# Kernel optimization log

Hardware: AMD Instinct MI355X
Metric: run time of the kernel (lower is better)

## Reference

```python
import jax, jax.numpy as jnp
import numpy as np

B, N, F, T, O, E = 4, 30000, 32, 12, 64, 480000


def setup_inputs() -> dict:
    key = jax.random.key(0)
    ks = jax.random.split(key, 20)
    s = 0.05
    inp = {
        "X": jax.random.normal(ks[0], (B, N, F, T), dtype=jnp.float32),
        "edge_index": jax.random.randint(ks[1], (2, E), 0, N, dtype=jnp.int64),
        # GCNConv weights for the three gates (num_layers=1 -> single conv each)
        "Wg_z": jax.random.normal(ks[2], (F, O), dtype=jnp.float32) * s,
        "bg_z": jnp.zeros((O,), jnp.float32),
        "Wg_r": jax.random.normal(ks[3], (F, O), dtype=jnp.float32) * s,
        "bg_r": jnp.zeros((O,), jnp.float32),
        "Wg_h": jax.random.normal(ks[4], (F, O), dtype=jnp.float32) * s,
        "bg_h": jnp.zeros((O,), jnp.float32),
        # gate Linear(2*O, O) weights
        "Wl_z": jax.random.normal(ks[5], (2 * O, O), dtype=jnp.float32) * s,
        "bl_z": jnp.zeros((O,), jnp.float32),
        "Wl_r": jax.random.normal(ks[6], (2 * O, O), dtype=jnp.float32) * s,
        "bl_r": jnp.zeros((O,), jnp.float32),
        "Wl_h": jax.random.normal(ks[7], (2 * O, O), dtype=jnp.float32) * s,
        "bl_h": jnp.zeros((O,), jnp.float32),
        # A3TGCN per-period attention and final readout Linear(O, T)
        "att": jax.random.normal(ks[8], (T,), dtype=jnp.float32),
        "W_out": jax.random.normal(ks[9], (O, T), dtype=jnp.float32) * s,
        "b_out": jnp.zeros((T,), jnp.float32),
    }
    return inp


def reference(X, edge_index, Wg_z, bg_z, Wg_r, bg_r, Wg_h, bg_h,
              Wl_z, bl_z, Wl_r, bl_r, Wl_h, bl_h, att, W_out, b_out):
    src, dst = edge_index[0], edge_index[1]
    n = X.shape[1]
    # GCN symmetric normalization with self-loops: deg = in-degree + 1
    deg = jnp.zeros((n,), X.dtype).at[dst].add(1.0) + 1.0
    dis = jax.lax.rsqrt(deg)  # deg^{-1/2}
    edge_norm = (dis[src] * dis[dst])[None, :, None]  # [1,E,1]
    self_norm = (dis * dis)[None, :, None]            # [1,N,1]

    def gcn_conv(x, W, b):  # x: [B,N,F] -> [B,N,O]
        xw = jnp.einsum('bnf,fo->bno', x, W)
        agg = jnp.zeros_like(xw).at[:, dst, :].add(xw[:, src, :] * edge_norm)
        return agg + xw * self_norm + b

    H0 = jnp.zeros((X.shape[0], n, Wg_z.shape[1]), X.dtype)  # H defaults to zeros
    probs = jax.nn.softmax(att)

    def step(acc, inp):
        x_t, p = inp  # x_t: [B,N,F]
        Z = jax.nn.sigmoid(jnp.concatenate([gcn_conv(x_t, Wg_z, bg_z), H0], -1) @ Wl_z + bl_z)
        R = jax.nn.sigmoid(jnp.concatenate([gcn_conv(x_t, Wg_r, bg_r), H0], -1) @ Wl_r + bl_r)
        Ht = jnp.tanh(jnp.concatenate([gcn_conv(x_t, Wg_h, bg_h), H0 * R], -1) @ Wl_h + bl_h)
        Hn = Z * H0 + (1.0 - Z) * Ht
        return acc + p * Hn, None

    Xt = jnp.moveaxis(X, -1, 0)  # [T,B,N,F]
    H_acc, _ = jax.lax.scan(step, jnp.zeros_like(H0), (Xt, probs))
    # TemporalGNN head: ReLU + Linear(O, periods)
    return jax.nn.relu(H_acc) @ W_out + b_out  # [B,N,T]
```

## Files before the change

kernel.cpp:

```cpp
#include <hip/hip_runtime.h>
#include <hip/hip_bf16.h>
#include <hip/hip_fp16.h>


#define FDIM 32
#define TDIM 12
#define ODIM 64
#define BDIM 4
#define SCAN_TILE 1024

typedef _Float16 half8v __attribute__((ext_vector_type(8)));
typedef float float4v __attribute__((ext_vector_type(4)));

__global__ __launch_bounds__(256) void kA(
    const float4* __restrict__ Xin, uint2* __restrict__ Xh, int n4, int cvtB,
    const int* __restrict__ dstE, int* __restrict__ counts, int E, int cntB,
    const float* __restrict__ Wg_z, const float* __restrict__ bg_z,
    const float* __restrict__ Wl_z, const float* __restrict__ bl_z,
    const float* __restrict__ Wg_h, const float* __restrict__ bg_h,
    const float* __restrict__ Wl_h, const float* __restrict__ bl_h,
    const float* __restrict__ att,
    float* __restrict__ Wz, float* __restrict__ bz,
    float* __restrict__ Wh, float* __restrict__ bh,
    float* __restrict__ probs) {
    const int bid = blockIdx.x;
    const int tid = threadIdx.x;
    if (bid < cvtB) {
        int i = bid * 256 + tid;
        const int stride = cvtB * 256;
        for (; i < n4; i += stride) {
            const float4 v = Xin[i];
            __half2 h0 = __floats2half2_rn(v.x, v.y);
            __half2 h1 = __floats2half2_rn(v.z, v.w);
            uint2 u;
            u.x = *reinterpret_cast<unsigned*>(&h0);
            u.y = *reinterpret_cast<unsigned*>(&h1);
            Xh[i] = u;
        }
    } else if (bid < cvtB + cntB) {
        int e = (bid - cvtB) * 256 + tid;
        if (e < E) atomicAdd(&counts[dstE[e]], 1);
    } else {
        for (int i = tid; i < FDIM * ODIM; i += 256) {
            int f = i >> 6, o = i & 63;
            float az = 0.f, ah = 0.f;
            for (int k = 0; k < ODIM; k++) {
                az += Wg_z[f * ODIM + k] * Wl_z[k * ODIM + o];
                ah += Wg_h[f * ODIM + k] * Wl_h[k * ODIM + o];
            }
            Wz[i] = az;
            Wh[i] = ah;
        }
        if (tid < ODIM) {
            float az = bl_z[tid], ah = bl_h[tid];
            for (int k = 0; k < ODIM; k++) {
                az += bg_z[k] * Wl_z[k * ODIM + tid];
                ah += bg_h[k] * Wl_h[k * ODIM + tid];
            }
            bz[tid] = az;
            bh[tid] = ah;
        }
        if (tid == 0) {
            float m = -1e30f;
            for (int t = 0; t < TDIM; t++) m = fmaxf(m, att[t]);
            float e[TDIM], s = 0.f;
            for (int t = 0; t < TDIM; t++) { e[t] = expf(att[t] - m); s += e[t]; }
            for (int t = 0; t < TDIM; t++) probs[t] = e[t] / s;
        }
    }
}

__global__ __launch_bounds__(256) void kB1(const int* __restrict__ counts, int N,
                                           int* __restrict__ partials) {
    __shared__ int wsum[4];
    const int tid = threadIdx.x;
    const int blk = blockIdx.x;
    const int i0 = blk * SCAN_TILE + tid * 4;
    int s = 0;
    s += (i0 + 0 < N) ? counts[i0 + 0] + 1 : 0;
    s += (i0 + 1 < N) ? counts[i0 + 1] + 1 : 0;
    s += (i0 + 2 < N) ? counts[i0 + 2] + 1 : 0;
    s += (i0 + 3 < N) ? counts[i0 + 3] + 1 : 0;
    for (int off = 1; off < 64; off <<= 1) s += __shfl_xor(s, off, 64);
    if ((tid & 63) == 0) wsum[tid >> 6] = s;
    __syncthreads();
    if (tid == 0) partials[blk] = wsum[0] + wsum[1] + wsum[2] + wsum[3];
}

__global__ __launch_bounds__(256) void kB3(const int* __restrict__ counts, int N,
                                           const int* __restrict__ partials,
                                           int* __restrict__ offsets,
                                           float* __restrict__ dis,
                                           int* __restrict__ fill,
                                           int2* __restrict__ csr, int E) {
    __shared__ int sBase;
    __shared__ int wsum[4];
    const int tid = threadIdx.x;
    const int blk = blockIdx.x;
    const int lane = tid & 63;
    const int wv = tid >> 6;

    if (tid == 0) {
        int acc = 0;
        for (int j = 0; j < blk; j++) acc += partials[j];
        sBase = acc;
    }

    const int i0 = blk * SCAN_TILE + tid * 4;
    const int e0 = (i0 + 0 < N) ? counts[i0 + 0] + 1 : 0;
    const int e1 = (i0 + 1 < N) ? counts[i0 + 1] + 1 : 0;
    const int e2 = (i0 + 2 < N) ? counts[i0 + 2] + 1 : 0;
    const int e3 = (i0 + 3 < N) ? counts[i0 + 3] + 1 : 0;
    const int s = e0 + e1 + e2 + e3;
    int inc = s;
    for (int off = 1; off < 64; off <<= 1) {
        int t = __shfl_up(inc, off, 64);
        if (lane >= off) inc += t;
    }
    if (lane == 63) wsum[wv] = inc;
    __syncthreads();
    int wbase = 0;
    for (int j = 0; j < wv; j++) wbase += wsum[j];
    int base = sBase + wbase + inc - s;

    const int ee[4] = {e0, e1, e2, e3};
#pragma unroll
    for (int k = 0; k < 4; k++) {
        const int i = i0 + k;
        if (i < N) {
            offsets[i] = base;
            const float d = 1.0f / sqrtf((float)ee[k]);
            dis[i] = d;
            fill[i] = 1;
            const float nm = d * d;
            __half2 mh = __floats2half2_rn(nm, nm);
            csr[base] = make_int2(i, *(int*)&mh);
            base += ee[k];
        }
    }
    if (blk == 0 && tid == 0) offsets[N] = E + N;
}

__global__ void k_scatter(const int* __restrict__ src, const int* __restrict__ dst,
                          const int* __restrict__ offsets, int* __restrict__ fill,
                          const float* __restrict__ dis,
                          int2* __restrict__ csr, int E) {
    int e = blockIdx.x * 256 + threadIdx.x;
    if (e < E) {
        int s = src[e], d = dst[e];
        int pos = offsets[d] + atomicAdd(&fill[d], 1);
        float nm = dis[s] * dis[d];
        __half2 mh = __floats2half2_rn(nm, nm);
        csr[pos] = make_int2(s, *(int*)&mh);
    }
}

__device__ __forceinline__ float sigm(float x) { return 1.f / (1.f + __expf(-x)); }
__device__ __forceinline__ float tanhfast(float x) { return 1.f - 2.f / (1.f + __expf(2.f * x)); }

#define HPACC(mhI, v, hs0, hs1, hs2, hs3)                                      \
    {                                                                          \
        int mi_ = (mhI);                                                       \
        __half2 mh_ = *(__half2*)&mi_;                                         \
        hs0 = __hfma2(mh_, *(__half2*)&(v).x, hs0);                            \
        hs1 = __hfma2(mh_, *(__half2*)&(v).y, hs1);                            \
        hs2 = __hfma2(mh_, *(__half2*)&(v).z, hs2);                            \
        hs3 = __hfma2(mh_, *(__half2*)&(v).w, hs3);                            \
    }

#define HFLUSH(hs0, hs1, hs2, hs3)                                             \
    {                                                                          \
        float2 t_;                                                             \
        t_ = __half22float2(hs0); a0 += t_.x; a1 += t_.y;                      \
        t_ = __half22float2(hs1); a2 += t_.x; a3 += t_.y;                      \
        t_ = __half22float2(hs2); a4 += t_.x; a5 += t_.y;                      \
        t_ = __half22float2(hs3); a6 += t_.x; a7 += t_.y;                      \
        hs0 = hzero; hs1 = hzero; hs2 = hzero; hs3 = hzero;                    \
    }

#define LOADB(dst, Wsrc, jt)                                                   \
    {                                                                          \
        _Pragma("unroll") for (int r_ = 0; r_ < 8; r_++)                       \
            dst[r_] = (_Float16)Wsrc[(kg * 8 + r_) * ODIM + (jt) * 16 + c];    \
    }

#define EPI(qv, dzv, dhv, bzv, bhv)                                            \
    {                                                                          \
        float s_ = 0.f;                                                        \
        {  const float zf_ = dzv[0] + bzv, hf_ = dhv[0] + bhv;                 \
           const float u_ = __expf(-zf_), v_ = __expf(2.f * hf_);              \
           s_ += pr0 * u_ * (v_ - 1.f) *                                       \
                 __builtin_amdgcn_rcpf((1.f + u_) * (1.f + v_)); }             \
        {  const float zf_ = dzv[1] + bzv, hf_ = dhv[1] + bhv;                 \
           const float u_ = __expf(-zf_), v_ = __expf(2.f * hf_);              \
           s_ += pr1 * u_ * (v_ - 1.f) *                                       \
                 __builtin_amdgcn_rcpf((1.f + u_) * (1.f + v_)); }             \
        {  const float zf_ = dzv[2] + bzv, hf_ = dhv[2] + bhv;                 \
           const float u_ = __expf(-zf_), v_ = __expf(2.f * hf_);              \
           s_ += pr2 * u_ * (v_ - 1.f) *                                       \
                 __builtin_amdgcn_rcpf((1.f + u_) * (1.f + v_)); }             \
        {  const float zf_ = dzv[3] + bzv, hf_ = dhv[3] + bhv;                 \
           const float u_ = __expf(-zf_), v_ = __expf(2.f * hf_);              \
           s_ += pr3 * u_ * (v_ - 1.f) *                                       \
                 __builtin_amdgcn_rcpf((1.f + u_) * (1.f + v_)); }             \
        s_ += __shfl_xor(s_, 16, 64);                                          \
        s_ += __shfl_xor(s_, 32, 64);                                          \
        qv = s_;                                                               \
    }

__global__ __launch_bounds__(256, 4) void k_main_w(
    const uint4* __restrict__ Xh, const int* __restrict__ offs,
    const int2* __restrict__ csr,
    const float* __restrict__ Wz, const float* __restrict__ bz,
    const float* __restrict__ Wh, const float* __restrict__ bh,
    const float* __restrict__ probs, const float* __restrict__ Wout,
    const float* __restrict__ bout, float* __restrict__ out, int N) {
    __shared__ float sY[4][16 * 36 + 4];

    const int tid = threadIdx.x;
    const int wv = tid >> 6;
    const int lane = tid & 63;
    const int lanec = lane < 47 ? lane : 47;
    const int c = lane & 15;
    const int kg = lane >> 4;

    half8v wzf0, wzf1, wzf2, wzf3, whf0, whf1, whf2, whf3;
    LOADB(wzf0, Wz, 0) LOADB(wzf1, Wz, 1) LOADB(wzf2, Wz, 2) LOADB(wzf3, Wz, 3)
    LOADB(whf0, Wh, 0) LOADB(whf1, Wh, 1) LOADB(whf2, Wh, 2) LOADB(whf3, Wh, 3)
    half8v wo0, wo1;
#pragma unroll
    for (int r_ = 0; r_ < 8; r_++) {
        wo0[r_] = (_Float16)((c < TDIM) ? Wout[(kg * 8 + r_) * TDIM + c] : 0.f);
        wo1[r_] = (_Float16)((c < TDIM) ? Wout[(32 + kg * 8 + r_) * TDIM + c] : 0.f);
    }
    const float bz0 = bz[c], bz1 = bz[16 + c], bz2 = bz[32 + c], bz3 = bz[48 + c];
    const float bh0 = bh[c], bh1 = bh[16 + c], bh2 = bh[32 + c], bh3 = bh[48 + c];
    const float pr0 = (kg * 4 + 0 < TDIM) ? probs[kg * 4 + 0] : 0.f;
    const float pr1 = (kg * 4 + 1 < TDIM) ? probs[kg * 4 + 1] : 0.f;
    const float pr2 = (kg * 4 + 2 < TDIM) ? probs[kg * 4 + 2] : 0.f;
    const float pr3 = (kg * 4 + 3 < TDIM) ? probs[kg * 4 + 3] : 0.f;
    const float bo = (lane < TDIM) ? bout[lane] : 0.f;
    const __half2 hzero = __float2half2_rn(0.f);

    float* __restrict__ sy = sY[wv];
    const int strideT = gridDim.x * 4;
    const int totalTasks = N * BDIM;

    int task0 = blockIdx.x * 4 + wv;
    if (task0 >= totalTasks) return;
    int b = task0 / N;
    int n = task0 - b * N;

    while (true) {
        const int bs = __builtin_amdgcn_readfirstlane(b);
        const int ns = __builtin_amdgcn_readfirstlane(n);
        const unsigned rowB = (unsigned)bs * (unsigned)N;
        const int begS = __builtin_amdgcn_readfirstlane(offs[ns]);
        const int endS = __builtin_amdgcn_readfirstlane(offs[ns + 1]);

        float a0 = 0.f, a1 = 0.f, a2 = 0.f, a3 = 0.f,
              a4 = 0.f, a5 = 0.f, a6 = 0.f, a7 = 0.f;
        __half2 hA0 = hzero, hA1 = hzero, hA2 = hzero, hA3 = hzero;
        __half2 hB0 = hzero, hB1 = hzero, hB2 = hzero, hB3 = hzero;
        int j = begS;
        for (; j + 8 <= endS; j += 8) {
            const int2 e0 = csr[j + 0], e1 = csr[j + 1], e2 = csr[j + 2], e3 = csr[j + 3];
            const int2 e4 = csr[j + 4], e5 = csr[j + 5], e6 = csr[j + 6], e7 = csr[j + 7];
            const uint4 x0 = Xh[(rowB + (unsigned)e0.x) * 48u + lanec];
            const uint4 x1 = Xh[(rowB + (unsigned)e1.x) * 48u + lanec];
            const uint4 x2 = Xh[(rowB + (unsigned)e2.x) * 48u + lanec];
            const uint4 x3 = Xh[(rowB + (unsigned)e3.x) * 48u + lanec];
            const uint4 x4 = Xh[(rowB + (unsigned)e4.x) * 48u + lanec];
            const uint4 x5 = Xh[(rowB + (unsigned)e5.x) * 48u + lanec];
            const uint4 x6 = Xh[(rowB + (unsigned)e6.x) * 48u + lanec];
            const uint4 x7 = Xh[(rowB + (unsigned)e7.x) * 48u + lanec];
            HPACC(e0.y, x0, hA0, hA1, hA2, hA3);
            HPACC(e1.y, x1, hA0, hA1, hA2, hA3);
            HPACC(e2.y, x2, hA0, hA1, hA2, hA3);
            HPACC(e3.y, x3, hA0, hA1, hA2, hA3);
            HPACC(e4.y, x4, hB0, hB1, hB2, hB3);
            HPACC(e5.y, x5, hB0, hB1, hB2, hB3);
            HPACC(e6.y, x6, hB0, hB1, hB2, hB3);
            HPACC(e7.y, x7, hB0, hB1, hB2, hB3);
            HFLUSH(hA0, hA1, hA2, hA3);
            HFLUSH(hB0, hB1, hB2, hB3);
        }
        for (; j < endS; ++j) {
            const int2 e = csr[j];
            const uint4 xv = Xh[(rowB + (unsigned)e.x) * 48u + lanec];
            HPACC(e.y, xv, hA0, hA1, hA2, hA3);
        }
        HFLUSH(hA0, hA1, hA2, hA3);

        if (lane < 48) {
            int flat = lane * 8;
            int f = flat / 12;
            int t = flat - f * 12;
#pragma unroll
            for (int k = 0; k < 8; k++) {
                float av = (k == 0) ? a0 : (k == 1) ? a1 : (k == 2) ? a2 :
                           (k == 3) ? a3 : (k == 4) ? a4 : (k == 5) ? a5 :
                           (k == 6) ? a6 : a7;
                sy[t * 36 + f] = av;
                t++;
                if (t == TDIM) { t = 0; f++; }
            }
        }

        half8v af;
        if (c < TDIM) {
            const float4* yp = (const float4*)&sy[c * 36 + kg * 8];
            const float4 y0 = yp[0];
            const float4 y1 = yp[1];
            af[0] = (_Float16)y0.x; af[1] = (_Float16)y0.y;
            af[2] = (_Float16)y0.z; af[3] = (_Float16)y0.w;
            af[4] = (_Float16)y1.x; af[5] = (_Float16)y1.y;
            af[6] = (_Float16)y1.z; af[7] = (_Float16)y1.w;
        } else {
            af[0] = (_Float16)0.f; af[1] = (_Float16)0.f;
            af[2] = (_Float16)0.f; af[3] = (_Float16)0.f;
            af[4] = (_Float16)0.f; af[5] = (_Float16)0.f;
            af[6] = (_Float16)0.f; af[7] = (_Float16)0.f;
        }

        const float4v zero4 = {0.f, 0.f, 0.f, 0.f};
        float4v dz0 = __builtin_amdgcn_mfma_f32_16x16x32_f16(af, wzf0, zero4, 0, 0, 0);
        float4v dz1 = __builtin_amdgcn_mfma_f32_16x16x32_f16(af, wzf1, zero4, 0, 0, 0);
        float4v dz2 = __builtin_amdgcn_mfma_f32_16x16x32_f16(af, wzf2, zero4, 0, 0, 0);
        float4v dz3 = __builtin_amdgcn_mfma_f32_16x16x32_f16(af, wzf3, zero4, 0, 0, 0);
        float4v dh0 = __builtin_amdgcn_mfma_f32_16x16x32_f16(af, whf0, zero4, 0, 0, 0);
        float4v dh1 = __builtin_amdgcn_mfma_f32_16x16x32_f16(af, whf1, zero4, 0, 0, 0);
        float4v dh2 = __builtin_amdgcn_mfma_f32_16x16x32_f16(af, whf2, zero4, 0, 0, 0);
        float4v dh3 = __builtin_amdgcn_mfma_f32_16x16x32_f16(af, whf3, zero4, 0, 0, 0);

        float q0, q1, q2, q3;
        EPI(q0, dz0, dh0, bz0, bh0)
        EPI(q1, dz1, dh1, bz1, bh1)
        EPI(q2, dz2, dh2, bz2, bh2)
        EPI(q3, dz3, dh3, bz3, bh3)
        const float accOwn = (kg == 0) ? q0 : (kg == 1) ? q1 : (kg == 2) ? q2 : q3;

        const float r = fmaxf(accOwn, 0.f);
        half8v ra0, ra1;
#pragma unroll
        for (int j2 = 0; j2 < 8; j2++) {
            ra0[j2] = (_Float16)__shfl(r, (kg << 3) + j2, 64);
            ra1[j2] = (_Float16)__shfl(r, 32 + (kg << 3) + j2, 64);
        }
        float4v dro = __builtin_amdgcn_mfma_f32_16x16x32_f16(ra0, wo0, zero4, 0, 0, 0);
        dro = __builtin_amdgcn_mfma_f32_16x16x32_f16(ra1, wo1, dro, 0, 0, 0);
        if (lane < TDIM)
            out[(rowB + (unsigned)n) * TDIM + lane] = dro[0] + bo;

        n += strideT;
        if (n >= N) { n -= N; b++; }
        if (b >= BDIM) break;
    }
}

__global__ __launch_bounds__(384) void k_main_f(
    const float* __restrict__ X, const int* __restrict__ offsets,
    const int2* __restrict__ csr, const float* __restrict__ dis,
    const float* __restrict__ Wz, const float* __restrict__ bz,
    const float* __restrict__ Wh, const float* __restrict__ bh,
    const float* __restrict__ probs, const float* __restrict__ Wout,
    const float* __restrict__ bout, float* __restrict__ out, int N) {
    const int tid = threadIdx.x;
    const int lane = tid & 63;

    __shared__ float4 sY4[BDIM][96];
    __shared__ float sAcc[BDIM][ODIM];
    __shared__ float sWout[ODIM * TDIM];
    __shared__ float sBout[TDIM];

    for (int i = tid; i < ODIM * TDIM; i += 384) sWout[i] = Wout[i];
    if (tid < TDIM) sBout[tid] = bout[tid];

    const int o = tid & 63;
    const int w = tid >> 6;
    float wzr[FDIM], whr[FDIM];
#pragma unroll
    for (int f = 0; f < FDIM; f++) {
        wzr[f] = Wz[f * ODIM + o];
        whr[f] = Wh[f * ODIM + o];
    }
    const float bzo = bz[o], bho = bh[o];
    const int t0 = w, t1 = w + 6;
    const float p0 = probs[t0], p1 = probs[t1];

    const int b = tid / 96;
    const int q = tid - b * 96;
    const float4* __restrict__ Xq = (const float4*)X;
    const unsigned rowBase = (unsigned)b * (unsigned)N;

    for (int n = blockIdx.x; n < N; n += gridDim.x) {
        if (tid < BDIM * ODIM) ((float*)sAcc)[tid] = 0.f;

        const int beg = offsets[n], end = offsets[n + 1];
        float4 A0 = make_float4(0.f, 0.f, 0.f, 0.f);
        float4 A1 = A0, A2 = A0, A3 = A0;

        for (int ebase = beg; ebase < end; ebase += 64) {
            const int cnt2 = min(64, end - ebase);
            int esrc = 0;
            float enm = 0.f;
            if (ebase + lane < end) {
                const int2 e = csr[ebase + lane];
                esrc = e.x;
                int ey = e.y;
                enm = __half22float2(*(__half2*)&ey).x;
            }
            int j = 0;
            for (; j + 4 <= cnt2; j += 4) {
                const int s0 = __shfl(esrc, j + 0, 64), s1 = __shfl(esrc, j + 1, 64);
                const int s2 = __shfl(esrc, j + 2, 64), s3 = __shfl(esrc, j + 3, 64);
                const float m0 = __shfl(enm, j + 0, 64), m1 = __shfl(enm, j + 1, 64);
                const float m2 = __shfl(enm, j + 2, 64), m3 = __shfl(enm, j + 3, 64);
                const float4 u0 = Xq[(rowBase + s0) * 96u + q];
                const float4 u1 = Xq[(rowBase + s1) * 96u + q];
                const float4 u2 = Xq[(rowBase + s2) * 96u + q];
                const float4 u3 = Xq[(rowBase + s3) * 96u + q];
                A0.x += m0 * u0.x; A0.y += m0 * u0.y; A0.z += m0 * u0.z; A0.w += m0 * u0.w;
                A1.x += m1 * u1.x; A1.y += m1 * u1.y; A1.z += m1 * u1.z; A1.w += m1 * u1.w;
                A2.x += m2 * u2.x; A2.y += m2 * u2.y; A2.z += m2 * u2.z; A2.w += m2 * u2.w;
                A3.x += m3 * u3.x; A3.y += m3 * u3.y; A3.z += m3 * u3.z; A3.w += m3 * u3.w;
            }
            for (; j < cnt2; j++) {
                const int s = __shfl(esrc, j, 64);
                const float m = __shfl(enm, j, 64);
                const float4 u = Xq[(rowBase + s) * 96u + q];
                A0.x += m * u.x; A0.y += m * u.y; A0.z += m * u.z; A0.w += m * u.w;
            }
        }
        A0.x += (A1.x + A2.x) + A3.x;
        A0.y += (A1.y + A2.y) + A3.y;
        A0.z += (A1.z + A2.z) + A3.z;
        A0.w += (A1.w + A2.w) + A3.w;
        sY4[b][q] = A0;
        __syncthreads();

#pragma unroll
        for (int bb = 0; bb < BDIM; bb++) {
            const float* yb = (const float*)sY4[bb];
            float z0 = bzo, z1 = bzo, h0 = bho, h1 = bho;
#pragma unroll
            for (int f = 0; f < FDIM; f++) {
                float ya = yb[f * TDIM + t0];
                float yc = yb[f * TDIM + t1];
                z0 += ya * wzr[f]; h0 += ya * whr[f];
                z1 += yc * wzr[f]; h1 += yc * whr[f];
            }
            float contrib = p0 * (1.f - sigm(z0)) * tanhfast(h0)
                          + p1 * (1.f - sigm(z1)) * tanhfast(h1);
            atomicAdd(&sAcc[bb][o], contrib);
        }
        __syncthreads();

        if (tid < BDIM * TDIM) {
            int ob = tid / TDIM, jj = tid - ob * TDIM;
            float v = sBout[jj];
#pragma unroll
            for (int o2 = 0; o2 < ODIM; o2++) {
                v += fmaxf(sAcc[ob][o2], 0.f) * sWout[o2 * TDIM + jj];
            }
            out[(unsigned)(ob * N + n) * TDIM + jj] = v;
        }
        __syncthreads();
    }
}

extern "C" void kernel_launch(void* const* d_in, const int* in_sizes, int n_in,
                              void* d_out, int out_size, void* d_ws, size_t ws_size,
                              hipStream_t stream) {
    const float* X    = (const float*)d_in[0];
    const int*   ei   = (const int*)d_in[1];
    const float* Wg_z = (const float*)d_in[2];
    const float* bg_z = (const float*)d_in[3];
    const float* Wg_h = (const float*)d_in[6];
    const float* bg_h = (const float*)d_in[7];
    const float* Wl_z = (const float*)d_in[8];
    const float* bl_z = (const float*)d_in[9];
    const float* Wl_h = (const float*)d_in[12];
    const float* bl_h = (const float*)d_in[13];
    const float* att  = (const float*)d_in[14];
    const float* Wout = (const float*)d_in[15];
    const float* bout = (const float*)d_in[16];
    float* out = (float*)d_out;

    const int E = in_sizes[1] / 2;
    const int N = in_sizes[0] / (BDIM * FDIM * TDIM);
    const size_t xElems = (size_t)BDIM * N * FDIM * TDIM;
    const size_t xhBytes = xElems * 2;
    const size_t csrBytes = (size_t)(E + N) * 8;
    const size_t restBytes = (size_t)N * 4 * 4 + 4096 + csrBytes + 20000;
    const bool useH = ws_size >= xhBytes + restBytes;
    const int nScanBlk = (N + SCAN_TILE - 1) / SCAN_TILE;

    char* wp = (char*)d_ws;
    uint2* Xh = nullptr;
    if (useH) { Xh = (uint2*)wp; wp += xhBytes; }
    int* counts   = (int*)wp;   wp += (size_t)N * 4;
    int* fill     = (int*)wp;   wp += (size_t)N * 4;
    int* offs     = (int*)wp;   wp += (size_t)(N + 4) * 4;
    float* dis    = (float*)wp; wp += (size_t)N * 4;
    int* partials = (int*)wp;   wp += (size_t)(nScanBlk + 4) * 4;
    int2* csr     = (int2*)wp;  wp += csrBytes;
    float* Wz     = (float*)wp; wp += FDIM * ODIM * 4;
    float* Wh     = (float*)wp; wp += FDIM * ODIM * 4;
    float* bz     = (float*)wp; wp += ODIM * 4;
    float* bh     = (float*)wp; wp += ODIM * 4;
    float* probs  = (float*)wp; wp += 16 * 4;

    hipMemsetAsync(counts, 0, (size_t)N * 4, stream);

    const int cvtB = useH ? 2048 : 0;
    const int cntB = (E + 255) / 256;
    const int n4 = (int)(xElems / 4);
    kA<<<cvtB + cntB + 1, 256, 0, stream>>>(
        (const float4*)X, Xh, n4, cvtB,
        ei + E, counts, E, cntB,
        Wg_z, bg_z, Wl_z, bl_z, Wg_h, bg_h, Wl_h, bl_h, att,
        Wz, bz, Wh, bh, probs);
    kB1<<<nScanBlk, 256, 0, stream>>>(counts, N, partials);
    kB3<<<nScanBlk, 256, 0, stream>>>(counts, N, partials, offs, dis, fill, csr, E);
    k_scatter<<<(E + 255) / 256, 256, 0, stream>>>(ei, ei + E, offs, fill, dis, csr, E);

    if (useH) {
        k_main_w<<<2048, 256, 0, stream>>>((const uint4*)Xh, offs, csr,
                                           Wz, bz, Wh, bh, probs, Wout, bout, out, N);
    } else {
        int nB = N < 2048 ? N : 2048;
        k_main_f<<<nB, 384, 0, stream>>>(X, offs, csr, dis, Wz, bz, Wh, bh,
                                         probs, Wout, bout, out, N);
    }
}
```

Before: 335.6 us.

## Fuse scan kernels, vectorize CSR loads, and prefetch next node offsets

Merges the two-pass prefix scan into one kernel in which each block redundantly sums all preceding counts itself, removing a launch and the partials buffer. The gather loop now reads CSR entries two at a time as int4 after peeling one entry to reach even alignment. It also loads the next task's offsets before the epilogue so that latency overlaps with compute. The cost is extra redundant count reads in the scan, since later blocks read more of the prefix, plus an added barrier.

Result: slower. 407.7 us (+21.5%).

```diff
diff --git a/kernel.cpp b/kernel.cpp
--- a/kernel.cpp
+++ b/kernel.cpp
@@ -70,29 +70,11 @@
     }
 }
 
-__global__ __launch_bounds__(256) void kB1(const int* __restrict__ counts, int N,
-                                           int* __restrict__ partials) {
-    __shared__ int wsum[4];
-    const int tid = threadIdx.x;
-    const int blk = blockIdx.x;
-    const int i0 = blk * SCAN_TILE + tid * 4;
-    int s = 0;
-    s += (i0 + 0 < N) ? counts[i0 + 0] + 1 : 0;
-    s += (i0 + 1 < N) ? counts[i0 + 1] + 1 : 0;
-    s += (i0 + 2 < N) ? counts[i0 + 2] + 1 : 0;
-    s += (i0 + 3 < N) ? counts[i0 + 3] + 1 : 0;
-    for (int off = 1; off < 64; off <<= 1) s += __shfl_xor(s, off, 64);
-    if ((tid & 63) == 0) wsum[tid >> 6] = s;
-    __syncthreads();
-    if (tid == 0) partials[blk] = wsum[0] + wsum[1] + wsum[2] + wsum[3];
-}
-
-__global__ __launch_bounds__(256) void kB3(const int* __restrict__ counts, int N,
-                                           const int* __restrict__ partials,
-                                           int* __restrict__ offsets,
-                                           float* __restrict__ dis,
-                                           int* __restrict__ fill,
-                                           int2* __restrict__ csr, int E) {
+__global__ __launch_bounds__(256) void kB(const int* __restrict__ counts, int N,
+                                          int* __restrict__ offsets,
+                                          float* __restrict__ dis,
+                                          int* __restrict__ fill,
+                                          int2* __restrict__ csr, int E) {
     __shared__ int sBase;
     __shared__ int wsum[4];
     const int tid = threadIdx.x;
@@ -100,11 +82,14 @@
     const int lane = tid & 63;
     const int wv = tid >> 6;
 
-    if (tid == 0) {
-        int acc = 0;
-        for (int j = 0; j < blk; j++) acc += partials[j];
-        sBase = acc;
-    }
+    int pre = 0;
+    const int preEnd = blk * SCAN_TILE;
+    for (int i = tid; i < preEnd; i += 256) pre += counts[i] + 1;
+    for (int off = 1; off < 64; off <<= 1) pre += __shfl_xor(pre, off, 64);
+    if (lane == 0) wsum[wv] = pre;
+    __syncthreads();
+    if (tid == 0) sBase = wsum[0] + wsum[1] + wsum[2] + wsum[3];
+    __syncthreads();
 
     const int i0 = blk * SCAN_TILE + tid * 4;
     const int e0 = (i0 + 0 < N) ? counts[i0 + 0] + 1 : 0;
@@ -117,6 +102,7 @@
         int t = __shfl_up(inc, off, 64);
         if (lane >= off) inc += t;
     }
+    __syncthreads();
     if (lane == 63) wsum[wv] = inc;
     __syncthreads();
     int wbase = 0;
@@ -241,6 +227,7 @@
     const float pr3 = (kg * 4 + 3 < TDIM) ? probs[kg * 4 + 3] : 0.f;
     const float bo = (lane < TDIM) ? bout[lane] : 0.f;
     const __half2 hzero = __float2half2_rn(0.f);
+    const int4* __restrict__ csr4 = (const int4*)csr;
 
     float* __restrict__ sy = sY[wv];
     const int strideT = gridDim.x * 4;
@@ -251,37 +238,50 @@
     int b = task0 / N;
     int n = task0 - b * N;
 
+    int begS, endS;
+    {
+        const int ns0 = __builtin_amdgcn_readfirstlane(n);
+        begS = __builtin_amdgcn_readfirstlane(offs[ns0]);
+        endS = __builtin_amdgcn_readfirstlane(offs[ns0 + 1]);
+    }
+
     while (true) {
         const int bs = __builtin_amdgcn_readfirstlane(b);
-        const int ns = __builtin_amdgcn_readfirstlane(n);
         const unsigned rowB = (unsigned)bs * (unsigned)N;
-        const int begS = __builtin_amdgcn_readfirstlane(offs[ns]);
-        const int endS = __builtin_amdgcn_readfirstlane(offs[ns + 1]);
 
         float a0 = 0.f, a1 = 0.f, a2 = 0.f, a3 = 0.f,
               a4 = 0.f, a5 = 0.f, a6 = 0.f, a7 = 0.f;
         __half2 hA0 = hzero, hA1 = hzero, hA2 = hzero, hA3 = hzero;
         __half2 hB0 = hzero, hB1 = hzero, hB2 = hzero, hB3 = hzero;
         int j = begS;
+        if ((j & 1) && j < endS) {
+            const int2 e = csr[j];
+            const uint4 xv = Xh[(rowB + (unsigned)e.x) * 48u + lanec];
+            HPACC(e.y, xv, hA0, hA1, hA2, hA3);
+            ++j;
+        }
         for (; j + 8 <= endS; j += 8) {
-            const int2 e0 = csr[j + 0], e1 = csr[j + 1], e2 = csr[j + 2], e3 = csr[j + 3];
-            const int2 e4 = csr[j + 4], e5 = csr[j + 5], e6 = csr[j + 6], e7 = csr[j + 7];
-            const uint4 x0 = Xh[(rowB + (unsigned)e0.x) * 48u + lanec];
-            const uint4 x1 = Xh[(rowB + (unsigned)e1.x) * 48u + lanec];
-            const uint4 x2 = Xh[(rowB + (unsigned)e2.x) * 48u + lanec];
-            const uint4 x3 = Xh[(rowB + (unsigned)e3.x) * 48u + lanec];
-            const uint4 x4 = Xh[(rowB + (unsigned)e4.x) * 48u + lanec];
-            const uint4 x5 = Xh[(rowB + (unsigned)e5.x) * 48u + lanec];
-            const uint4 x6 = Xh[(rowB + (unsigned)e6.x) * 48u + lanec];
-            const uint4 x7 = Xh[(rowB + (unsigned)e7.x) * 48u + lanec];
-            HPACC(e0.y, x0, hA0, hA1, hA2, hA3);
-            HPACC(e1.y, x1, hA0, hA1, hA2, hA3);
-            HPACC(e2.y, x2, hA0, hA1, hA2, hA3);
-            HPACC(e3.y, x3, hA0, hA1, hA2, hA3);
-            HPACC(e4.y, x4, hB0, hB1, hB2, hB3);
-            HPACC(e5.y, x5, hB0, hB1, hB2, hB3);
-            HPACC(e6.y, x6, hB0, hB1, hB2, hB3);
-            HPACC(e7.y, x7, hB0, hB1, hB2, hB3);
+            const int jh = j >> 1;
+            const int4 p0 = csr4[jh + 0];
+            const int4 p1 = csr4[jh + 1];
+            const int4 p2 = csr4[jh + 2];
+            const int4 p3 = csr4[jh + 3];
+            const uint4 x0 = Xh[(rowB + (unsigned)p0.x) * 48u + lanec];
+            const uint4 x1 = Xh[(rowB + (unsigned)p0.z) * 48u + lanec];
+            const uint4 x2 = Xh[(rowB + (unsigned)p1.x) * 48u + lanec];
+            const uint4 x3 = Xh[(rowB + (unsigned)p1.z) * 48u + lanec];
+            const uint4 x4 = Xh[(rowB + (unsigned)p2.x) * 48u + lanec];
+            const uint4 x5 = Xh[(rowB + (unsigned)p2.z) * 48u + lanec];
+            const uint4 x6 = Xh[(rowB + (unsigned)p3.x) * 48u + lanec];
+            const uint4 x7 = Xh[(rowB + (unsigned)p3.z) * 48u + lanec];
+            HPACC(p0.y, x0, hA0, hA1, hA2, hA3);
+            HPACC(p0.w, x1, hA0, hA1, hA2, hA3);
+            HPACC(p1.y, x2, hA0, hA1, hA2, hA3);
+            HPACC(p1.w, x3, hA0, hA1, hA2, hA3);
+            HPACC(p2.y, x4, hB0, hB1, hB2, hB3);
+            HPACC(p2.w, x5, hB0, hB1, hB2, hB3);
+            HPACC(p3.y, x6, hB0, hB1, hB2, hB3);
+            HPACC(p3.w, x7, hB0, hB1, hB2, hB3);
             HFLUSH(hA0, hA1, hA2, hA3);
             HFLUSH(hB0, hB1, hB2, hB3);
         }
@@ -291,6 +291,16 @@
             HPACC(e.y, xv, hA0, hA1, hA2, hA3);
         }
         HFLUSH(hA0, hA1, hA2, hA3);
+
+        int nn = n + strideT, nb = b;
+        if (nn >= N) { nn -= N; nb++; }
+        const bool hasNext = nb < BDIM;
+        int begN = 0, endN = 0;
+        if (hasNext) {
+            const int nns = __builtin_amdgcn_readfirstlane(nn);
+            begN = __builtin_amdgcn_readfirstlane(offs[nns]);
+            endN = __builtin_amdgcn_readfirstlane(offs[nns + 1]);
+        }
 
         if (lane < 48) {
             int flat = lane * 8;
@@ -352,9 +362,8 @@
         if (lane < TDIM)
             out[(rowB + (unsigned)n) * TDIM + lane] = dro[0] + bo;
 
-        n += strideT;
-        if (n >= N) { n -= N; b++; }
-        if (b >= BDIM) break;
+        if (!hasNext) break;
+        b = nb; n = nn; begS = begN; endS = endN;
     }
 }
 
@@ -503,7 +512,6 @@
     int* fill     = (int*)wp;   wp += (size_t)N * 4;
     int* offs     = (int*)wp;   wp += (size_t)(N + 4) * 4;
     float* dis    = (float*)wp; wp += (size_t)N * 4;
-    int* partials = (int*)wp;   wp += (size_t)(nScanBlk + 4) * 4;
     int2* csr     = (int2*)wp;  wp += csrBytes;
     float* Wz     = (float*)wp; wp += FDIM * ODIM * 4;
     float* Wh     = (float*)wp; wp += FDIM * ODIM * 4;
@@ -521,8 +529,7 @@
         ei + E, counts, E, cntB,
         Wg_z, bg_z, Wl_z, bl_z, Wg_h, bg_h, Wl_h, bl_h, att,
         Wz, bz, Wh, bh, probs);
-    kB1<<<nScanBlk, 256, 0, stream>>>(counts, N, partials);
-    kB3<<<nScanBlk, 256, 0, stream>>>(counts, N, partials, offs, dis, fill, csr, E);
+    kB<<<nScanBlk, 256, 0, stream>>>(counts, N, offs, dis, fill, csr, E);
     k_scatter<<<(E + 255) / 256, 256, 0, stream>>>(ei, ei + E, offs, fill, dis, csr, E);
 
     if (useH) {
```
